# Performance work log

Measured on AMD Instinct MI355X. Metric: run time of the kernel, lower is better.

Reference implementation:

```python
import jax, jax.numpy as jnp
import numpy as np

B, N, DIM = 4, 4096, 512
HEADS, DH = 8, 64          # dim_head = dim // 8
M = 256                    # num_landmarks = dim // 2
ITERS = 6                  # pinv iterations
K = 33                     # residual depthwise conv kernel
INNER = HEADS * DH


def setup_inputs() -> dict:
    key = jax.random.key(0)
    ks = jax.random.split(key, 7)
    return {
        "x": jax.random.normal(ks[0], (B, N, DIM), jnp.float32),
        "norm_w": 1.0 + 0.02 * jax.random.normal(ks[1], (DIM,), jnp.float32),
        "norm_b": 0.02 * jax.random.normal(ks[2], (DIM,), jnp.float32),
        "w_qkv": jax.random.normal(ks[3], (DIM, 3 * INNER), jnp.float32) / np.sqrt(DIM),
        "w_out": jax.random.normal(ks[4], (INNER, DIM), jnp.float32) / np.sqrt(INNER),
        "b_out": 0.02 * jax.random.normal(ks[5], (DIM,), jnp.float32),
        "res_w": jax.random.normal(ks[6], (HEADS, 1, K, 1), jnp.float32) / np.sqrt(K),
    }


def _moore_penrose_pinv(x, iters):
    # iterative Newton-Schulz pseudoinverse, as in lucidrains nystrom-attention
    abs_x = jnp.abs(x)
    col = abs_x.sum(-1)
    row = abs_x.sum(-2)
    z = jnp.swapaxes(x, -1, -2) / (jnp.max(col) * jnp.max(row))
    I = jnp.eye(x.shape[-1], dtype=x.dtype)
    for _ in range(iters):
        xz = x @ z
        z = 0.25 * z @ (13.0 * I - xz @ (15.0 * I - xz @ (7.0 * I - xz)))
    return z


def reference(x, norm_w, norm_b, w_qkv, w_out, b_out, res_w):
    # LayerNorm (eps=1e-5, torch default)
    mu = x.mean(-1, keepdims=True)
    var = ((x - mu) ** 2).mean(-1, keepdims=True)
    xn = (x - mu) / jnp.sqrt(var + 1e-5) * norm_w + norm_b

    qkv = xn @ w_qkv                               # [B,N,3*INNER]
    q, k, v = jnp.split(qkv, 3, axis=-1)
    to_heads = lambda t: t.reshape(B, N, HEADS, DH).transpose(0, 2, 1, 3)  # [B,H,N,D]
    q, k, v = to_heads(q), to_heads(k), to_heads(v)
    q = q * (DH ** -0.5)

    # landmarks: mean over consecutive blocks of l = N // M tokens
    l = N // M
    q_l = q.reshape(B, HEADS, M, l, DH).mean(3)    # [B,H,M,D]
    k_l = k.reshape(B, HEADS, M, l, DH).mean(3)

    sim1 = jnp.einsum('bhid,bhjd->bhij', q, k_l)   # [B,H,N,M]
    sim2 = jnp.einsum('bhid,bhjd->bhij', q_l, k_l) # [B,H,M,M]
    sim3 = jnp.einsum('bhid,bhjd->bhij', q_l, k)   # [B,H,M,N]
    a1 = jax.nn.softmax(sim1, -1)
    a2 = jax.nn.softmax(sim2, -1)
    a3 = jax.nn.softmax(sim3, -1)

    a2_inv = _moore_penrose_pinv(a2, ITERS)
    out = (a1 @ a2_inv) @ (a3 @ v)                 # [B,H,N,D]

    # residual depthwise conv over sequence dim (Conv2d(h,h,(33,1),groups=h))
    out = out + jax.lax.conv_general_dilated(
        v, res_w, (1, 1), ((K // 2, K // 2), (0, 0)),
        feature_group_count=HEADS,
        dimension_numbers=('NCHW', 'OIHW', 'NCHW'))

    out = out.transpose(0, 2, 1, 3).reshape(B, N, INNER)
    out = out @ w_out + b_out                      # to_out (dropout inactive at eval)
    return x + out                                 # TransLayer residual
```

## Files before the change

kernel.cpp:

```cpp
#include <hip/hip_runtime.h>
#include <math.h>

typedef unsigned short u16;
typedef short s16x8 __attribute__((ext_vector_type(8)));
typedef float f32x4 __attribute__((ext_vector_type(4)));

#define MFMA16(a, b, c) __builtin_amdgcn_mfma_f32_16x16x32_bf16((a), (b), (c), 0, 0, 0)

__device__ __forceinline__ u16 f2b(float f) {
  unsigned u = __float_as_uint(f);
  unsigned r = (u + 0x7fff + ((u >> 16) & 1)) >> 16;
  return (u16)r;
}
__device__ __forceinline__ float b2f(u16 h) { return __uint_as_float(((unsigned)h) << 16); }

__global__ __launch_bounds__(256) void prep_kernel(const float* __restrict__ x, const float* __restrict__ w,
    const float* __restrict__ b, u16* __restrict__ xn,
    const float* __restrict__ Wq, u16* __restrict__ WqT,
    const float* __restrict__ Wo, u16* __restrict__ WoT,
    unsigned* __restrict__ scal) {
  int bI = blockIdx.x;
  int t = threadIdx.x;
  if (bI == 0 && t == 0) { scal[0] = 0u; scal[1] = 0u; }
  if (bI < 16384) {
    int row = bI;
    const float* xr = x + (size_t)row * 512;
    float v0 = xr[t], v1 = xr[t + 256];
    float s = v0 + v1, ss = v0*v0 + v1*v1;
    for (int o = 32; o > 0; o >>= 1) { s += __shfl_down(s, o); ss += __shfl_down(ss, o); }
    __shared__ float ls[4], lss[4];
    int wid = t >> 6, lane = t & 63;
    if (lane == 0) { ls[wid] = s; lss[wid] = ss; }
    __syncthreads();
    float tot  = ls[0]+ls[1]+ls[2]+ls[3];
    float tot2 = lss[0]+lss[1]+lss[2]+lss[3];
    float mean = tot * (1.f/512);
    float var  = tot2 * (1.f/512) - mean*mean;
    float inv = rsqrtf(var + 1e-5f);
    u16* xo = xn + (size_t)row * 512;
    xo[t]     = f2b((v0-mean)*inv*w[t]     + b[t]);
    xo[t+256] = f2b((v1-mean)*inv*w[t+256] + b[t+256]);
  } else if (bI < 16384 + 3072) {
    int idx = (bI - 16384)*256 + t;
    int r = idx / 1536, c = idx - r*1536;
    WqT[(size_t)c*512 + r] = f2b(Wq[idx]);
  } else {
    int idx = (bI - 19456)*256 + t;
    int r = idx >> 9, c = idx & 511;
    WoT[(size_t)c*512 + r] = f2b(Wo[idx]);
  }
}

__device__ __forceinline__ void gemm128_pf(const u16* __restrict__ A, const u16* __restrict__ BT,
    int K, int ldA, int ldBT, int row0, int col0, u16* As, u16* Bs, f32x4 acc[4][4]) {
  int t = threadIdx.x, lane = t & 63, wid = t >> 6;
  int wr = (wid >> 1) * 64, wc = (wid & 1) * 64;
  int lr = lane & 15, lg = lane >> 4;
  int sr = t >> 2, sc = (t & 3) * 8;
  const u16* Ar0 = A  + (size_t)(row0 + sr)*ldA + sc;
  const u16* Ar1 = A  + (size_t)(row0 + sr + 64)*ldA + sc;
  const u16* Br0 = BT + (size_t)(col0 + sr)*ldBT + sc;
  const u16* Br1 = BT + (size_t)(col0 + sr + 64)*ldBT + sc;
  uint4 pa0 = *(const uint4*)Ar0, pa1 = *(const uint4*)Ar1;
  uint4 pb0 = *(const uint4*)Br0, pb1 = *(const uint4*)Br1;
  for (int k0 = 0; k0 < K; k0 += 32) {
    __syncthreads();
    *(uint4*)&As[sr*40 + sc]        = pa0;
    *(uint4*)&As[(sr + 64)*40 + sc] = pa1;
    *(uint4*)&Bs[sr*40 + sc]        = pb0;
    *(uint4*)&Bs[(sr + 64)*40 + sc] = pb1;
    __syncthreads();
    if (k0 + 32 < K) {
      pa0 = *(const uint4*)(Ar0 + k0 + 32);
      pa1 = *(const uint4*)(Ar1 + k0 + 32);
      pb0 = *(const uint4*)(Br0 + k0 + 32);
      pb1 = *(const uint4*)(Br1 + k0 + 32);
    }
    s16x8 af[4], bf[4];
    #pragma unroll
    for (int f = 0; f < 4; f++) {
      af[f] = *(s16x8*)&As[(wr + f*16 + lr)*40 + lg*8];
      bf[f] = *(s16x8*)&Bs[(wc + f*16 + lr)*40 + lg*8];
    }
    #pragma unroll
    for (int i = 0; i < 4; i++)
      #pragma unroll
      for (int j = 0; j < 4; j++)
        acc[i][j] = MFMA16(af[i], bf[j], acc[i][j]);
  }
}

__device__ __forceinline__ void gemm64_pf(const u16* __restrict__ Ab, const u16* __restrict__ Bb,
    int row0, int col0, u16* As, u16* Bs, f32x4 acc[2][2]) {
  int t = threadIdx.x, lane = t & 63, wid = t >> 6;
  int wr = (wid >> 1)*32, wc = (wid & 1)*32;
  int lr = lane & 15, lg = lane >> 4;
  int sr = t >> 3, sc = (t & 7)*8;
  const u16* Ar0 = Ab + (size_t)(row0 + sr)*256 + sc;
  const u16* Ar1 = Ab + (size_t)(row0 + 32 + sr)*256 + sc;
  const u16* Br0 = Bb + (size_t)(col0 + sr)*256 + sc;
  const u16* Br1 = Bb + (size_t)(col0 + 32 + sr)*256 + sc;
  uint4 pa0 = *(const uint4*)Ar0, pa1 = *(const uint4*)Ar1;
  uint4 pb0 = *(const uint4*)Br0, pb1 = *(const uint4*)Br1;
  for (int k0 = 0; k0 < 256; k0 += 64) {
    __syncthreads();
    *(uint4*)&As[sr*72 + sc]        = pa0;
    *(uint4*)&As[(sr + 32)*72 + sc] = pa1;
    *(uint4*)&Bs[sr*72 + sc]        = pb0;
    *(uint4*)&Bs[(sr + 32)*72 + sc] = pb1;
    __syncthreads();
    if (k0 + 64 < 256) {
      pa0 = *(const uint4*)(Ar0 + k0 + 64);
      pa1 = *(const uint4*)(Ar1 + k0 + 64);
      pb0 = *(const uint4*)(Br0 + k0 + 64);
      pb1 = *(const uint4*)(Br1 + k0 + 64);
    }
    #pragma unroll
    for (int kk = 0; kk < 2; kk++) {
      s16x8 af[2], bf[2];
      #pragma unroll
      for (int f = 0; f < 2; f++) {
        af[f] = *(s16x8*)&As[(wr + f*16 + lr)*72 + kk*32 + lg*8];
        bf[f] = *(s16x8*)&Bs[(wc + f*16 + lr)*72 + kk*32 + lg*8];
      }
      #pragma unroll
      for (int i = 0; i < 2; i++)
        #pragma unroll
        for (int j = 0; j < 2; j++)
          acc[i][j] = MFMA16(af[i], bf[j], acc[i][j]);
    }
  }
}

__global__ __launch_bounds__(256, 4) void qkv_mfma(const u16* __restrict__ xn, const u16* __restrict__ wT,
    u16* __restrict__ q, u16* __restrict__ k, u16* __restrict__ v,
    u16* __restrict__ ql, u16* __restrict__ kl) {
  __shared__ u16 As[128*40], Bs[128*40];
  f32x4 acc[4][4];
  #pragma unroll
  for (int i = 0; i < 4; i++)
    #pragma unroll
    for (int j = 0; j < 4; j++) acc[i][j] = (f32x4)0.f;
  int bI = blockIdx.x;
  int job = (bI & 7)*192 + (bI >> 3);
  int row0 = (job / 12) * 128, col0 = (job % 12) * 128;
  gemm128_pf(xn, wT, 512, 512, 512, row0, col0, As, Bs, acc);
  int t = threadIdx.x, lane = t & 63, wid = t >> 6, lr = lane & 15, lg = lane >> 4;
  int wr = (wid >> 1)*64, wc = (wid & 1)*64;
  int part = col0 >> 9;
  #pragma unroll
  for (int i = 0; i < 4; i++)
    #pragma unroll
    for (int j = 0; j < 4; j++)
      #pragma unroll
      for (int r = 0; r < 4; r++) {
        int row = row0 + wr + i*16 + lg*4 + r;
        int col = col0 + wc + j*16 + lr;
        float val = acc[i][j][r];
        int rem = col & 511, h = rem >> 6, d = rem & 63;
        int b = row >> 12, n = row & 4095;
        size_t bh = (size_t)(b*8 + h);
        size_t dst = (bh*4096 + n)*64 + d;
        if (part == 0)      q[dst] = f2b(val * 0.125f);
        else if (part == 1) k[dst] = f2b(val);
        else                v[dst] = f2b(val);
      }
  if (part <= 1) {
    #pragma unroll
    for (int i = 0; i < 4; i++) {
      #pragma unroll
      for (int j = 0; j < 4; j++) {
        float s = acc[i][j][0] + acc[i][j][1] + acc[i][j][2] + acc[i][j][3];
        s += __shfl_xor(s, 16);
        s += __shfl_xor(s, 32);
        if (lg == 0) {
          int row16 = row0 + wr + i*16;
          int b = row16 >> 12, n = row16 & 4095;
          int m = n >> 4;
          int col = col0 + wc + j*16 + lr;
          int rem = col & 511, h = rem >> 6, d = rem & 63;
          size_t dst = ((size_t)(b*8 + h)*256 + m)*64 + d;
          if (part == 0) ql[dst] = f2b(s * (0.125f/16.f));
          else           kl[dst] = f2b(s * (1.f/16.f));
        }
      }
    }
  }
}

__global__ __launch_bounds__(256, 4) void out_mfma(const u16* __restrict__ outh, const u16* __restrict__ wT,
    const float* __restrict__ bo, const float* __restrict__ x, float* __restrict__ out) {
  __shared__ u16 As[128*40], Bs[128*40];
  f32x4 acc[4][4];
  #pragma unroll
  for (int i = 0; i < 4; i++)
    #pragma unroll
    for (int j = 0; j < 4; j++) acc[i][j] = (f32x4)0.f;
  int bI = blockIdx.x;
  int job = (bI & 7)*64 + (bI >> 3);
  int row0 = (job / 4) * 128, col0 = (job % 4) * 128;
  gemm128_pf(outh, wT, 512, 512, 512, row0, col0, As, Bs, acc);
  int t = threadIdx.x, lane = t & 63, wid = t >> 6, lr = lane & 15, lg = lane >> 4;
  int wr = (wid >> 1)*64, wc = (wid & 1)*64;
  #pragma unroll
  for (int i = 0; i < 4; i++)
    #pragma unroll
    for (int j = 0; j < 4; j++)
      #pragma unroll
      for (int r = 0; r < 4; r++) {
        int row = row0 + wr + i*16 + lg*4 + r;
        int col = col0 + wc + j*16 + lr;
        size_t idx = (size_t)row*512 + col;
        out[idx] = x[idx] + acc[i][j][r] + bo[col];
      }
}

__global__ __launch_bounds__(256) void mid_kernel(
    const u16* __restrict__ v, u16* __restrict__ vT,
    const u16* __restrict__ ql, const u16* __restrict__ kl,
    u16* __restrict__ a2h, float* __restrict__ pcs,
    const float* __restrict__ rw, u16* __restrict__ outh) {
  __shared__ __align__(16) u16 smem[25600];
  int bI = blockIdx.x;
  int t = threadIdx.x;
  if (bI < 128) {
    int rq = bI & 3, bh = bI >> 2;
    u16* Qs  = smem;
    u16* Ks2 = smem + 4608;
    float* wcol = (float*)(smem + 23040);
    int lane = t & 63, wid = t >> 6, lr = lane & 15, lg = lane >> 4;
    #pragma unroll
    for (int p = 0; p < 2; p++) {
      int c = t + p*256;
      int r = c >> 3, col = (c & 7)*8;
      *(uint4*)&Qs[r*72 + col] = *(const uint4*)&ql[((size_t)bh*256 + rq*64 + r)*64 + col];
    }
    #pragma unroll
    for (int p = 0; p < 8; p++) {
      int c = t + p*256;
      int r = c >> 3, col = (c & 7)*8;
      *(uint4*)&Ks2[r*72 + col] = *(const uint4*)&kl[((size_t)bh*256 + r)*64 + col];
    }
    __syncthreads();
    float colp[16];
    #pragma unroll
    for (int cf = 0; cf < 16; cf++) colp[cf] = 0.f;
    int rbase = wid*16;
    s16x8 a0 = *(s16x8*)&Qs[(rbase + lr)*72 + lg*8];
    s16x8 a1 = *(s16x8*)&Qs[(rbase + lr)*72 + 32 + lg*8];
    f32x4 sf[16];
    #pragma unroll
    for (int cf = 0; cf < 16; cf++) {
      s16x8 b0 = *(s16x8*)&Ks2[(cf*16 + lr)*72 + lg*8];
      s16x8 b1 = *(s16x8*)&Ks2[(cf*16 + lr)*72 + 32 + lg*8];
      sf[cf] = MFMA16(a1, b1, MFMA16(a0, b0, (f32x4)0.f));
    }
    #pragma unroll
    for (int r = 0; r < 4; r++) {
      float mx = -3e38f;
      #pragma unroll
      for (int cf = 0; cf < 16; cf++) mx = fmaxf(mx, sf[cf][r]);
      #pragma unroll
      for (int o = 1; o < 16; o <<= 1) mx = fmaxf(mx, __shfl_xor(mx, o));
      float sum = 0.f;
      #pragma unroll
      for (int cf = 0; cf < 16; cf++) { sf[cf][r] = __expf(sf[cf][r] - mx); sum += sf[cf][r]; }
      #pragma unroll
      for (int o = 1; o < 16; o <<= 1) sum += __shfl_xor(sum, o);
      float inv = 1.f / sum;
      int row = rq*64 + rbase + lg*4 + r;
      size_t base = (size_t)bh*65536 + (size_t)row*256;
      #pragma unroll
      for (int cf = 0; cf < 16; cf++) {
        float pp = sf[cf][r] * inv;
        a2h[base + cf*16 + lr] = f2b(pp);
        colp[cf] += pp;
      }
    }
    #pragma unroll
    for (int cf = 0; cf < 16; cf++) {
      colp[cf] += __shfl_xor(colp[cf], 16);
      colp[cf] += __shfl_xor(colp[cf], 32);
    }
    if (lg == 0) {
      #pragma unroll
      for (int cf = 0; cf < 16; cf++) wcol[wid*256 + cf*16 + lr] = colp[cf];
    }
    __syncthreads();
    pcs[((size_t)bh*4 + rq)*256 + t] = wcol[t] + wcol[256 + t] + wcol[512 + t] + wcol[768 + t];
  } else if (bI < 2176) {
    int idx = bI - 128;
    int bh = idx >> 6, n0 = (idx & 63) * 64;
    u16* tile = smem;
    const u16* vb = v + ((size_t)bh*4096 + n0)*64;
    #pragma unroll
    for (int p = 0; p < 2; p++) {
      int c = t + p*256;
      int r = c >> 3, col = (c & 7)*8;
      *(uint4*)&tile[r*72 + col] = *(const uint4*)&vb[(size_t)r*64 + col];
    }
    __syncthreads();
    #pragma unroll
    for (int p = 0; p < 2; p++) {
      int c = t + p*256;
      int d = c >> 3, ncol = (c & 7)*8;
      u16 tmp[8];
      #pragma unroll
      for (int j = 0; j < 8; j++) tmp[j] = tile[(ncol + j)*72 + d];
      *(uint4*)&vT[((size_t)bh*64 + d)*4096 + n0 + ncol] = *(uint4*)tmp;
    }
  } else {
    int idx = bI - 2176;
    int bh = idx >> 5, n0 = (idx & 31) * 128;
    int b = bh >> 3, h = bh & 7;
    u16* tile = smem;
    float* wsm = (float*)(smem + 11520);
    if (t < 33) wsm[t] = rw[h*33 + t];
    const u16* vb = v + ((size_t)bh*4096)*64;
    #pragma unroll
    for (int p = 0; p < 5; p++) {
      int c = t + p*256;
      int r = c >> 3, col = (c & 7)*8;
      int nn = n0 - 16 + r;
      uint4 val = make_uint4(0u,0u,0u,0u);
      if (nn >= 0 && nn < 4096) val = *(const uint4*)&vb[(size_t)nn*64 + col];
      *(uint4*)&tile[r*72 + col] = val;
    }
    __syncthreads();
    int d8 = (t & 7) * 8;
    int r0 = t >> 3;
    #pragma unroll
    for (int pass = 0; pass < 4; pass++) {
      int lrow = pass*32 + r0;
      float acc[8] = {};
      #pragma unroll
      for (int j = 0; j < 33; j++) {
        uint4 vv = *(uint4*)&tile[(lrow + j)*72 + d8];
        float w = wsm[j];
        acc[0] += b2f((u16)(vv.x & 0xffff)) * w;
        acc[1] += b2f((u16)(vv.x >> 16))    * w;
        acc[2] += b2f((u16)(vv.y & 0xffff)) * w;
        acc[3] += b2f((u16)(vv.y >> 16))    * w;
        acc[4] += b2f((u16)(vv.z & 0xffff)) * w;
        acc[5] += b2f((u16)(vv.z >> 16))    * w;
        acc[6] += b2f((u16)(vv.w & 0xffff)) * w;
        acc[7] += b2f((u16)(vv.w >> 16))    * w;
      }
      size_t oi = ((size_t)(b*4096 + n0 + lrow))*512 + h*64 + d8;
      uint4 nv;
      nv.x = (unsigned)f2b(acc[0]) | ((unsigned)f2b(acc[1]) << 16);
      nv.y = (unsigned)f2b(acc[2]) | ((unsigned)f2b(acc[3]) << 16);
      nv.z = (unsigned)f2b(acc[4]) | ((unsigned)f2b(acc[5]) << 16);
      nv.w = (unsigned)f2b(acc[6]) | ((unsigned)f2b(acc[7]) << 16);
      *(uint4*)&outh[oi] = nv;
    }
  }
}

__global__ __launch_bounds__(256) void fp_cm(const u16* __restrict__ Q, const u16* __restrict__ Kg,
    const u16* __restrict__ VT, u16* __restrict__ po, float* __restrict__ pl,
    const float* __restrict__ pcs, unsigned* __restrict__ scal) {
  __shared__ __align__(16) u16 smem[13824];
  int bI = blockIdx.x;
  int t = threadIdx.x;
  if (bI >= 512) {
    float* red = (float*)smem;
    int bh = bI - 512;
    size_t b4 = (size_t)bh*4*256;
    red[t] = pcs[b4 + t] + pcs[b4 + 256 + t] + pcs[b4 + 512 + t] + pcs[b4 + 768 + t];
    __syncthreads();
    for (int o = 128; o > 0; o >>= 1) {
      if (t < o) red[t] = fmaxf(red[t], red[t+o]);
      __syncthreads();
    }
    if (t == 0) atomicMax(scal + 1, __float_as_uint(red[0]));
    return;
  }
  int ch = bI & 7, qg = (bI >> 3) & 1, bh = bI >> 4;
  u16* Ks = smem;
  u16* Vs = smem + 4608;
  u16* Ps = smem + 9216;
  int lane = t & 63, wid = t >> 6, lr = lane & 15, lg = lane >> 4;
  const u16* Qb  = Q  + ((size_t)bh*256)*64;
  const u16* Kb  = Kg + ((size_t)bh*4096 + ch*512)*64;
  const u16* VTb = VT + ((size_t)bh*64)*4096 + ch*512;
  s16x8 aq[2][2];
  #pragma unroll
  for (int qq = 0; qq < 2; qq++) {
    int qrow = (qg*2 + qq)*64 + wid*16 + lr;
    aq[qq][0] = *(const s16x8*)&Qb[(size_t)qrow*64 + lg*8];
    aq[qq][1] = *(const s16x8*)&Qb[(size_t)qrow*64 + 32 + lg*8];
  }
  f32x4 oacc[2][4];
  f32x4 lacc[2];
  #pragma unroll
  for (int qq = 0; qq < 2; qq++) {
    lacc[qq] = (f32x4)0.f;
    #pragma unroll
    for (int f = 0; f < 4; f++) oacc[qq][f] = (f32x4)0.f;
  }
  u16* Pw = Ps + wid*16*72;
  uint4 pk[2], pv[2];
  #pragma unroll
  for (int p = 0; p < 2; p++) {
    int c = t + p*256; int r = c >> 3, cc = (c & 7)*8;
    pk[p] = *(const uint4*)&Kb[(size_t)r*64 + cc];
    pv[p] = *(const uint4*)&VTb[(size_t)r*4096 + cc];
  }
  for (int k0 = 0; k0 < 512; k0 += 64) {
    __syncthreads();
    #pragma unroll
    for (int p = 0; p < 2; p++) {
      int c = t + p*256; int r = c >> 3, cc = (c & 7)*8;
      *(uint4*)&Ks[r*72 + cc] = pk[p];
      *(uint4*)&Vs[r*72 + cc] = pv[p];
    }
    __syncthreads();
    if (k0 + 64 < 512) {
      #pragma unroll
      for (int p = 0; p < 2; p++) {
        int c = t + p*256; int r = c >> 3, cc = (c & 7)*8;
        pk[p] = *(const uint4*)&Kb[(size_t)(k0 + 64 + r)*64 + cc];
        pv[p] = *(const uint4*)&VTb[(size_t)r*4096 + k0 + 64 + cc];
      }
    }
    #pragma unroll
    for (int qq = 0; qq < 2; qq++) {
      f32x4 sf[4];
      #pragma unroll
      for (int f = 0; f < 4; f++) {
        s16x8 b0 = *(s16x8*)&Ks[(f*16 + lr)*72 + lg*8];
        s16x8 b1 = *(s16x8*)&Ks[(f*16 + lr)*72 + 32 + lg*8];
        f32x4 s = (f32x4)0.f;
        s = MFMA16(aq[qq][0], b0, s);
        s = MFMA16(aq[qq][1], b1, s);
        sf[f] = s;
      }
      #pragma unroll
      for (int r = 0; r < 4; r++) {
        #pragma unroll
        for (int f = 0; f < 4; f++) {
          float pv2 = __expf(sf[f][r] - 8.f);
          lacc[qq][r] += pv2;
          Pw[(lg*4 + r)*72 + f*16 + lr] = f2b(pv2);
        }
      }
      #pragma unroll
      for (int ks = 0; ks < 2; ks++) {
        s16x8 ap = *(s16x8*)&Pw[lr*72 + ks*32 + lg*8];
        #pragma unroll
        for (int df = 0; df < 4; df++) {
          s16x8 bv = *(s16x8*)&Vs[(df*16 + lr)*72 + ks*32 + lg*8];
          oacc[qq][df] = MFMA16(ap, bv, oacc[qq][df]);
        }
      }
    }
  }
  #pragma unroll
  for (int qq = 0; qq < 2; qq++) {
    #pragma unroll
    for (int r = 0; r < 4; r++) {
      float s = lacc[qq][r];
      #pragma unroll
      for (int o = 1; o < 16; o <<= 1) s += __shfl_xor(s, o);
      lacc[qq][r] = s;
    }
  }
  #pragma unroll
  for (int qq = 0; qq < 2; qq++) {
    int pidx = (bh*4 + qg*2 + qq)*8 + ch;
    #pragma unroll
    for (int r = 0; r < 4; r++) {
      int lrow = wid*16 + lg*4 + r;
      if (lr == 0) pl[pidx*64 + lrow] = lacc[qq][r];
      uint2 pw2;
      pw2.x = (unsigned)f2b(oacc[qq][0][r]) | ((unsigned)f2b(oacc[qq][1][r]) << 16);
      pw2.y = (unsigned)f2b(oacc[qq][2][r]) | ((unsigned)f2b(oacc[qq][3][r]) << 16);
      *(uint2*)&po[((size_t)pidx*64 + lrow)*64 + lr*4] = pw2;
    }
  }
}

__global__ __launch_bounds__(256) void merge_z0(const u16* __restrict__ po,
    const float* __restrict__ pl, u16* __restrict__ a3vT,
    const u16* __restrict__ a2h, const unsigned* __restrict__ scal,
    u16* __restrict__ zA, u16* __restrict__ zAT) {
  __shared__ u16 tile[64*72];
  int bI = blockIdx.x;
  int t = threadIdx.x;
  if (bI < 128) {
    int qt = bI & 3, bh = bI >> 2;
    int lrow = t & 63, dg = t >> 6;
    int pbase = (bh*4 + qt)*8;
    float L = 0.f;
    #pragma unroll
    for (int ch = 0; ch < 8; ch++) L += pl[(pbase+ch)*64 + lrow];
    float Oacc[16];
    #pragma unroll
    for (int ss = 0; ss < 16; ss++) Oacc[ss] = 0.f;
    #pragma unroll
    for (int ch = 0; ch < 8; ch++) {
      const u16* pr = &po[(((size_t)(pbase+ch)*64 + lrow)*64) + dg*16];
      uint4 v0 = *(const uint4*)pr;
      uint4 v1 = *(const uint4*)(pr + 8);
      unsigned arr[8] = {v0.x, v0.y, v0.z, v0.w, v1.x, v1.y, v1.z, v1.w};
      #pragma unroll
      for (int jj = 0; jj < 8; jj++) {
        Oacc[jj*2]   += b2f((u16)(arr[jj] & 0xffff));
        Oacc[jj*2+1] += b2f((u16)(arr[jj] >> 16));
      }
    }
    float Linv = 1.f / L;
    #pragma unroll
    for (int ss = 0; ss < 16; ss++) {
      int s = dg*16 + ss;
      int c = ((s & 3) << 4) | (s >> 2);
      tile[c*72 + lrow] = f2b(Oacc[ss] * Linv);
    }
    __syncthreads();
    #pragma unroll
    for (int p = 0; p < 2; p++) {
      int idx = t + p*256;
      int d = idx >> 3, seg = idx & 7;
      u16 tmp[8];
      #pragma unroll
      for (int j = 0; j < 8; j++) tmp[j] = tile[d*72 + seg*8 + j];
      *(uint4*)&a3vT[((size_t)bh*64 + d)*256 + qt*64 + seg*8] = *(uint4*)tmp;
    }
  } else {
    size_t idx = (size_t)(bI - 128)*256 + t;
    float inv = 1.f / __uint_as_float(scal[1]);
    size_t bh = idx >> 16; int rem = (int)(idx & 65535); int i = rem >> 8, j = rem & 255;
    zA[idx]  = f2b(b2f(a2h[(bh<<16) + ((size_t)j<<8) + i]) * inv);
    zAT[idx] = f2b(b2f(a2h[idx]) * inv);
  }
}

__global__ __launch_bounds__(256) void pinv_s1(const u16* __restrict__ a2h, const u16* __restrict__ zcT,
    u16* __restrict__ xz, u16* __restrict__ xzT, u16* __restrict__ e1T) {
  __shared__ u16 As[64*72], Bs[64*72];
  size_t bb = (size_t)blockIdx.z << 16;
  f32x4 acc[2][2];
  #pragma unroll
  for (int i = 0; i < 2; i++) { acc[i][0] = (f32x4)0.f; acc[i][1] = (f32x4)0.f; }
  int row0 = blockIdx.y*64, col0 = blockIdx.x*64;
  gemm64_pf(a2h + bb, zcT + bb, row0, col0, As, Bs, acc);
  int t = threadIdx.x, lane = t & 63, wid = t >> 6, lr = lane & 15, lg = lane >> 4;
  int wr = (wid >> 1)*32, wc = (wid & 1)*32;
  #pragma unroll
  for (int i = 0; i < 2; i++)
    #pragma unroll
    for (int j = 0; j < 2; j++)
      #pragma unroll
      for (int r = 0; r < 4; r++) {
        int row = row0 + wr + i*16 + lg*4 + r;
        int col = col0 + wc + j*16 + lr;
        float c = acc[i][j][r];
        xz [bb + (size_t)row*256 + col] = f2b(c);
        xzT[bb + (size_t)col*256 + row] = f2b(c);
        e1T[bb + (size_t)col*256 + row] = f2b((row == col ? 7.f : 0.f) - c);
      }
}

__global__ __launch_bounds__(256) void pinv_s2(const u16* __restrict__ xz, const u16* __restrict__ e1T,
    const u16* __restrict__ zc, const u16* __restrict__ xzT,
    u16* __restrict__ e2T, u16* __restrict__ W) {
  __shared__ u16 As[64*72], Bs[64*72];
  int bz = blockIdx.z;
  bool isQ = bz < 32;
  size_t bb = (size_t)(isQ ? bz : bz - 32) << 16;
  const u16* Aptr = (isQ ? xz : zc) + bb;
  const u16* Bptr = (isQ ? e1T : xzT) + bb;
  f32x4 acc[2][2];
  #pragma unroll
  for (int i = 0; i < 2; i++) { acc[i][0] = (f32x4)0.f; acc[i][1] = (f32x4)0.f; }
  int row0 = blockIdx.y*64, col0 = blockIdx.x*64;
  gemm64_pf(Aptr, Bptr, row0, col0, As, Bs, acc);
  int t = threadIdx.x, lane = t & 63, wid = t >> 6, lr = lane & 15, lg = lane >> 4;
  int wr = (wid >> 1)*32, wc = (wid & 1)*32;
  #pragma unroll
  for (int i = 0; i < 2; i++)
    #pragma unroll
    for (int j = 0; j < 2; j++)
      #pragma unroll
      for (int r = 0; r < 4; r++) {
        int row = row0 + wr + i*16 + lg*4 + r;
        int col = col0 + wc + j*16 + lr;
        float c = acc[i][j][r];
        if (isQ) e2T[bb + (size_t)col*256 + row] = f2b((row == col ? 15.f : 0.f) - c);
        else     W  [bb + (size_t)row*256 + col] = f2b(c);
      }
}

__global__ __launch_bounds__(256) void pinv_s3(const u16* __restrict__ W, const u16* __restrict__ e2T,
    const u16* __restrict__ zc, u16* __restrict__ zn, u16* __restrict__ znT) {
  __shared__ u16 As[64*72], Bs[64*72];
  size_t bb = (size_t)blockIdx.z << 16;
  f32x4 acc[2][2];
  #pragma unroll
  for (int i = 0; i < 2; i++) { acc[i][0] = (f32x4)0.f; acc[i][1] = (f32x4)0.f; }
  int row0 = blockIdx.y*64, col0 = blockIdx.x*64;
  gemm64_pf(W + bb, e2T + bb, row0, col0, As, Bs, acc);
  int t = threadIdx.x, lane = t & 63, wid = t >> 6, lr = lane & 15, lg = lane >> 4;
  int wr = (wid >> 1)*32, wc = (wid & 1)*32;
  #pragma unroll
  for (int i = 0; i < 2; i++)
    #pragma unroll
    for (int j = 0; j < 2; j++)
      #pragma unroll
      for (int r = 0; r < 4; r++) {
        int row = row0 + wr + i*16 + lg*4 + r;
        int col = col0 + wc + j*16 + lr;
        size_t idx = bb + (size_t)row*256 + col;
        float val = 3.25f*b2f(zc[idx]) - 0.25f*acc[i][j][r];
        zn [idx] = f2b(val);
        znT[bb + (size_t)col*256 + row] = f2b(val);
      }
}

__global__ __launch_bounds__(256) void bmm64(const u16* __restrict__ A, const u16* __restrict__ BT,
    u16* __restrict__ CT, int M, int N, int K) {
  __shared__ u16 As[64*40], Bs[64*40];
  int batch = blockIdx.z;
  const u16* Ab = A  + (size_t)batch*M*K;
  const u16* Bb = BT + (size_t)batch*N*K;
  int row0 = blockIdx.y*64, col0 = blockIdx.x*64;
  int t = threadIdx.x, lane = t & 63, wid = t >> 6, lr = lane & 15, lg = lane >> 4;
  int wr = (wid >> 1)*32, wc = (wid & 1)*32;
  int sr = t >> 2, sc = (t & 3)*8;
  const u16* Arow = Ab + (size_t)(row0 + sr)*K + sc;
  const u16* Brow = Bb + (size_t)(col0 + sr)*K + sc;
  uint4 pa = *(const uint4*)Arow;
  uint4 pb = *(const uint4*)Brow;
  f32x4 acc[2][2];
  #pragma unroll
  for (int i = 0; i < 2; i++)
    #pragma unroll
    for (int j = 0; j < 2; j++) acc[i][j] = (f32x4)0.f;
  for (int k0 = 0; k0 < K; k0 += 32) {
    __syncthreads();
    *(uint4*)&As[sr*40 + sc] = pa;
    *(uint4*)&Bs[sr*40 + sc] = pb;
    __syncthreads();
    if (k0 + 32 < K) {
      pa = *(const uint4*)(Arow + k0 + 32);
      pb = *(const uint4*)(Brow + k0 + 32);
    }
    s16x8 af[2], bf[2];
    #pragma unroll
    for (int f = 0; f < 2; f++) {
      af[f] = *(s16x8*)&As[(wr + f*16 + lr)*40 + lg*8];
      bf[f] = *(s16x8*)&Bs[(wc + f*16 + lr)*40 + lg*8];
    }
    #pragma unroll
    for (int i = 0; i < 2; i++)
      #pragma unroll
      for (int j = 0; j < 2; j++)
        acc[i][j] = MFMA16(af[i], bf[j], acc[i][j]);
  }
  size_t cb = (size_t)batch*M*N;
  #pragma unroll
  for (int i = 0; i < 2; i++)
    #pragma unroll
    for (int j = 0; j < 2; j++)
      #pragma unroll
      for (int r = 0; r < 4; r++) {
        int row = row0 + wr + i*16 + lg*4 + r;
        int col = col0 + wc + j*16 + lr;
        CT[cb + (size_t)col*M + row] = f2b(acc[i][j][r]);
      }
}

__global__ __launch_bounds__(256, 4) void flash_a1(const u16* __restrict__ Q, const u16* __restrict__ Kl,
    const u16* __restrict__ W2T, u16* __restrict__ outh) {
  __shared__ u16 Ks[64*72];
  __shared__ u16 Vs[64*264];
  __shared__ u16 Ps[4*16*264];
  int bh = blockIdx.y;
  int q0 = blockIdx.x * 64;
  int t = threadIdx.x, lane = t & 63, wid = t >> 6, lr = lane & 15, lg = lane >> 4;
  const u16* Qb = Q + ((size_t)bh*4096)*64;
  #pragma unroll
  for (int p = 0; p < 8; p++) {
    int c = t + p*256; int r = c >> 5, col = (c & 31)*8;
    *(uint4*)&Vs[r*264 + col] = *(const uint4*)&W2T[((size_t)bh*64 + r)*256 + col];
  }
  int qrow = q0 + wid*16 + lr;
  s16x8 aq0 = *(const s16x8*)&Qb[(size_t)qrow*64 + lg*8];
  s16x8 aq1 = *(const s16x8*)&Qb[(size_t)qrow*64 + 32 + lg*8];
  f32x4 sf[16];
  #pragma unroll
  for (int f = 0; f < 16; f++) sf[f] = (f32x4)0.f;
  #pragma unroll
  for (int kt = 0; kt < 4; kt++) {
    __syncthreads();
    #pragma unroll
    for (int p = 0; p < 2; p++) {
      int c = t + p*256; int r = c >> 3, cc = (c & 7)*8;
      *(uint4*)&Ks[r*72 + cc] = *(const uint4*)&Kl[((size_t)bh*256 + kt*64 + r)*64 + cc];
    }
    __syncthreads();
    #pragma unroll
    for (int f2 = 0; f2 < 4; f2++) {
      s16x8 b0 = *(s16x8*)&Ks[(f2*16 + lr)*72 + lg*8];
      s16x8 b1 = *(s16x8*)&Ks[(f2*16 + lr)*72 + 32 + lg*8];
      sf[kt*4 + f2] = MFMA16(aq1, b1, MFMA16(aq0, b0, sf[kt*4 + f2]));
    }
  }
  u16* Pw = Ps + wid*16*264;
  float linv[4];
  #pragma unroll
  for (int r = 0; r < 4; r++) {
    float sum = 0.f;
    #pragma unroll
    for (int f = 0; f < 16; f++) {
      float pv = __expf(sf[f][r] - 8.f);
      sum += pv;
      Pw[(lg*4 + r)*264 + f*16 + lr] = f2b(pv);
    }
    #pragma unroll
    for (int o = 1; o < 16; o <<= 1) sum += __shfl_xor(sum, o);
    linv[r] = 1.f / sum;
  }
  f32x4 oacc[4];
  #pragma unroll
  for (int f = 0; f < 4; f++) oacc[f] = (f32x4)0.f;
  #pragma unroll
  for (int ks = 0; ks < 8; ks++) {
    s16x8 ap = *(s16x8*)&Pw[lr*264 + ks*32 + lg*8];
    #pragma unroll
    for (int df = 0; df < 4; df++) {
      s16x8 bv = *(s16x8*)&Vs[(df*16 + lr)*264 + ks*32 + lg*8];
      oacc[df] = MFMA16(ap, bv, oacc[df]);
    }
  }
  int b = bh >> 3, h = bh & 7;
  #pragma unroll
  for (int df = 0; df < 4; df++)
    #pragma unroll
    for (int r = 0; r < 4; r++) {
      int lrow = wid*16 + lg*4 + r;
      int col = df*16 + lr;
      size_t oi = ((size_t)(b*4096 + q0 + lrow))*512 + h*64 + col;
      outh[oi] = f2b(b2f(outh[oi]) + oacc[df][r] * linv[r]);
    }
}

extern "C" void kernel_launch(void* const* d_in, const int* in_sizes, int n_in,
                              void* d_out, int out_size, void* d_ws, size_t ws_size,
                              hipStream_t stream) {
  const float* x      = (const float*)d_in[0];
  const float* norm_w = (const float*)d_in[1];
  const float* norm_b = (const float*)d_in[2];
  const float* w_qkv  = (const float*)d_in[3];
  const float* w_out  = (const float*)d_in[4];
  const float* b_out  = (const float*)d_in[5];
  const float* res_w  = (const float*)d_in[6];
  float* out = (float*)d_out;
  char* ws = (char*)d_ws;

  size_t off = 0;
  u16* xn    = (u16*)(ws + off); off += 16777216;
  u16* q     = (u16*)(ws + off); off += 16777216;
  u16* k     = (u16*)(ws + off); off += 16777216;
  u16* v     = (u16*)(ws + off); off += 16777216;
  u16* vT    = (u16*)(ws + off); off += 16777216;
  u16* ql    = (u16*)(ws + off); off += 1048576;
  u16* kl    = (u16*)(ws + off); off += 1048576;
  u16* a2h   = (u16*)(ws + off); off += 4194304;
  u16* zA    = (u16*)(ws + off); off += 4194304;
  u16* zAT   = (u16*)(ws + off); off += 4194304;
  u16* zB    = (u16*)(ws + off); off += 4194304;
  u16* zBT   = (u16*)(ws + off); off += 4194304;
  u16* xz    = (u16*)(ws + off); off += 4194304;
  u16* xzT   = (u16*)(ws + off); off += 4194304;
  u16* e1T   = (u16*)(ws + off); off += 4194304;
  u16* e2T   = (u16*)(ws + off); off += 4194304;
  u16* Wm    = (u16*)(ws + off); off += 4194304;
  u16* a3vT  = (u16*)(ws + off); off += 1048576;
  u16* w2T   = (u16*)(ws + off); off += 1048576;
  u16* wqkvT = (u16*)(ws + off); off += 1572864;
  u16* woutT = (u16*)(ws + off); off += 524288;
  u16* outh  = (u16*)(ws + off); off += 16777216;
  u16* po    = (u16*)(ws + off); off += 8388608;
  float* pl  = (float*)(ws + off); off += 262144;
  float* pcs = (float*)(ws + off); off += 131072;
  unsigned* scal = (unsigned*)(ws + off); off += 8;

  prep_kernel<<<20480, 256, 0, stream>>>(x, norm_w, norm_b, xn, w_qkv, wqkvT, w_out, woutT, scal);
  qkv_mfma<<<1536, 256, 0, stream>>>(xn, wqkvT, q, k, v, ql, kl);
  mid_kernel<<<3200, 256, 0, stream>>>(v, vT, ql, kl, a2h, pcs, res_w, outh);
  fp_cm<<<544, 256, 0, stream>>>(ql, k, vT, po, pl, pcs, scal);
  merge_z0<<<8320, 256, 0, stream>>>(po, pl, a3vT, a2h, scal, zA, zAT);

  u16 *zc = zA, *zcT = zAT, *zn = zB, *znT = zBT;
  for (int it = 0; it < 6; it++) {
    pinv_s1<<<dim3(4,4,32), 256, 0, stream>>>(a2h, zcT, xz, xzT, e1T);
    pinv_s2<<<dim3(4,4,64), 256, 0, stream>>>(xz, e1T, zc, xzT, e2T, Wm);
    pinv_s3<<<dim3(4,4,32), 256, 0, stream>>>(Wm, e2T, zc, zn, znT);
    u16* tp;
    tp = zc; zc = zn; zn = tp;
    tp = zcT; zcT = znT; znT = tp;
  }

  bmm64<<<dim3(1,4,32), 256, 0, stream>>>(zc, a3vT, w2T, 256, 64, 256);
  flash_a1<<<dim3(64, 32), 256, 0, stream>>>(q, kl, w2T, outh);
  out_mfma<<<512, 256, 0, stream>>>(outh, woutT, b_out, x, out);
}
```

Measured before the change: 383.8 us.

## Fold z0 scaling into pinv stages and overlap flash/merge with pinv launches

Writes the transposed landmark softmax directly from mid_kernel and applies the 1/(max col*max row) scale inside the first pinv iteration, removing the merge_z0 elementwise pass. The a3·v partial flash blocks and their merge are fused as extra blocks into the first two pinv_s1 launches, so that independent work fills the otherwise underused GPU during the small pinv GEMMs. The column-max reduction moves to its own tiny kernel. This adds mode branching and larger shared-memory footprints to pinv_s1.

```diff
diff --git a/kernel.cpp b/kernel.cpp
--- a/kernel.cpp
+++ b/kernel.cpp
@@ -218,7 +218,7 @@
 __global__ __launch_bounds__(256) void mid_kernel(
     const u16* __restrict__ v, u16* __restrict__ vT,
     const u16* __restrict__ ql, const u16* __restrict__ kl,
-    u16* __restrict__ a2h, float* __restrict__ pcs,
+    u16* __restrict__ a2h, u16* __restrict__ a2hT, float* __restrict__ pcs,
     const float* __restrict__ rw, u16* __restrict__ outh) {
   __shared__ __align__(16) u16 smem[25600];
   int bI = blockIdx.x;
@@ -227,6 +227,7 @@
     int rq = bI & 3, bh = bI >> 2;
     u16* Qs  = smem;
     u16* Ks2 = smem + 4608;
+    u16* Pt  = smem;
     float* wcol = (float*)(smem + 23040);
     int lane = t & 63, wid = t >> 6, lr = lane & 15, lg = lane >> 4;
     #pragma unroll
@@ -255,6 +256,7 @@
       s16x8 b1 = *(s16x8*)&Ks2[(cf*16 + lr)*72 + 32 + lg*8];
       sf[cf] = MFMA16(a1, b1, MFMA16(a0, b0, (f32x4)0.f));
     }
+    float invs[4];
     #pragma unroll
     for (int r = 0; r < 4; r++) {
       float mx = -3e38f;
@@ -268,6 +270,7 @@
       #pragma unroll
       for (int o = 1; o < 16; o <<= 1) sum += __shfl_xor(sum, o);
       float inv = 1.f / sum;
+      invs[r] = inv;
       int row = rq*64 + rbase + lg*4 + r;
       size_t base = (size_t)bh*65536 + (size_t)row*256;
       #pragma unroll
@@ -288,6 +291,22 @@
     }
     __syncthreads();
     pcs[((size_t)bh*4 + rq)*256 + t] = wcol[t] + wcol[256 + t] + wcol[512 + t] + wcol[768 + t];
+    #pragma unroll
+    for (int cf = 0; cf < 16; cf++) {
+      int col = cf*16 + lr;
+      #pragma unroll
+      for (int r = 0; r < 4; r++) {
+        int lrow = rbase + lg*4 + r;
+        Pt[col*72 + lrow] = f2b(sf[cf][r] * invs[r]);
+      }
+    }
+    __syncthreads();
+    #pragma unroll
+    for (int p = 0; p < 8; p++) {
+      int c = t + p*256;
+      int j = c >> 3, o8 = (c & 7)*8;
+      *(uint4*)&a2hT[(size_t)bh*65536 + (size_t)j*256 + rq*64 + o8] = *(uint4*)&Pt[j*72 + o8];
+    }
   } else if (bI < 2176) {
     int idx = bI - 128;
     int bh = idx >> 6, n0 = (idx & 63) * 64;
@@ -357,29 +376,53 @@
   }
 }
 
-__global__ __launch_bounds__(256) void fp_cm(const u16* __restrict__ Q, const u16* __restrict__ Kg,
-    const u16* __restrict__ VT, u16* __restrict__ po, float* __restrict__ pl,
-    const float* __restrict__ pcs, unsigned* __restrict__ scal) {
-  __shared__ __align__(16) u16 smem[13824];
-  int bI = blockIdx.x;
-  int t = threadIdx.x;
-  if (bI >= 512) {
-    float* red = (float*)smem;
-    int bh = bI - 512;
-    size_t b4 = (size_t)bh*4*256;
-    red[t] = pcs[b4 + t] + pcs[b4 + 256 + t] + pcs[b4 + 512 + t] + pcs[b4 + 768 + t];
-    __syncthreads();
-    for (int o = 128; o > 0; o >>= 1) {
-      if (t < o) red[t] = fmaxf(red[t], red[t+o]);
-      __syncthreads();
-    }
-    if (t == 0) atomicMax(scal + 1, __float_as_uint(red[0]));
-    return;
-  }
-  int ch = bI & 7, qg = (bI >> 3) & 1, bh = bI >> 4;
+__global__ __launch_bounds__(256) void colmax_kernel(const float* __restrict__ pcs, unsigned* __restrict__ scal) {
+  __shared__ float red[256];
+  int bh = blockIdx.x, t = threadIdx.x;
+  size_t b4 = (size_t)bh*4*256;
+  red[t] = pcs[b4 + t] + pcs[b4 + 256 + t] + pcs[b4 + 512 + t] + pcs[b4 + 768 + t];
+  __syncthreads();
+  for (int o = 128; o > 0; o >>= 1) {
+    if (t < o) red[t] = fmaxf(red[t], red[t+o]);
+    __syncthreads();
+  }
+  if (t == 0) atomicMax(scal + 1, __float_as_uint(red[0]));
+}
+
+__device__ __forceinline__ void s1_body(int bI, u16* As, u16* Bs,
+    const u16* __restrict__ a2h, const u16* __restrict__ zcT,
+    u16* __restrict__ xz, u16* __restrict__ xzT, u16* __restrict__ e1T, float sc) {
+  size_t bb = (size_t)(bI >> 4) << 16;
+  int row0 = ((bI >> 2) & 3)*64, col0 = (bI & 3)*64;
+  f32x4 acc[2][2];
+  #pragma unroll
+  for (int i = 0; i < 2; i++) { acc[i][0] = (f32x4)0.f; acc[i][1] = (f32x4)0.f; }
+  gemm64_pf(a2h + bb, zcT + bb, row0, col0, As, Bs, acc);
+  int t = threadIdx.x, lane = t & 63, wid = t >> 6, lr = lane & 15, lg = lane >> 4;
+  int wr = (wid >> 1)*32, wc = (wid & 1)*32;
+  #pragma unroll
+  for (int i = 0; i < 2; i++)
+    #pragma unroll
+    for (int j = 0; j < 2; j++)
+      #pragma unroll
+      for (int r = 0; r < 4; r++) {
+        int row = row0 + wr + i*16 + lg*4 + r;
+        int col = col0 + wc + j*16 + lr;
+        float c = acc[i][j][r] * sc;
+        xz [bb + (size_t)row*256 + col] = f2b(c);
+        xzT[bb + (size_t)col*256 + row] = f2b(c);
+        e1T[bb + (size_t)col*256 + row] = f2b((row == col ? 7.f : 0.f) - c);
+      }
+}
+
+__device__ __forceinline__ void flash_body(int f, u16* smem,
+    const u16* __restrict__ Q, const u16* __restrict__ Kg, const u16* __restrict__ VT,
+    u16* __restrict__ po, float* __restrict__ pl) {
   u16* Ks = smem;
   u16* Vs = smem + 4608;
   u16* Ps = smem + 9216;
+  int t = threadIdx.x;
+  int ch = f & 7, qg = (f >> 3) & 1, bh = f >> 4;
   int lane = t & 63, wid = t >> 6, lr = lane & 15, lg = lane >> 4;
   const u16* Qb  = Q  + ((size_t)bh*256)*64;
   const u16* Kb  = Kg + ((size_t)bh*4096 + ch*512)*64;
@@ -397,7 +440,7 @@
   for (int qq = 0; qq < 2; qq++) {
     lacc[qq] = (f32x4)0.f;
     #pragma unroll
-    for (int f = 0; f < 4; f++) oacc[qq][f] = (f32x4)0.f;
+    for (int ff = 0; ff < 4; ff++) oacc[qq][ff] = (f32x4)0.f;
   }
   u16* Pw = Ps + wid*16*72;
   uint4 pk[2], pv[2];
@@ -428,21 +471,21 @@
     for (int qq = 0; qq < 2; qq++) {
       f32x4 sf[4];
       #pragma unroll
-      for (int f = 0; f < 4; f++) {
-        s16x8 b0 = *(s16x8*)&Ks[(f*16 + lr)*72 + lg*8];
-        s16x8 b1 = *(s16x8*)&Ks[(f*16 + lr)*72 + 32 + lg*8];
+      for (int ff = 0; ff < 4; ff++) {
+        s16x8 b0 = *(s16x8*)&Ks[(ff*16 + lr)*72 + lg*8];
+        s16x8 b1 = *(s16x8*)&Ks[(ff*16 + lr)*72 + 32 + lg*8];
         f32x4 s = (f32x4)0.f;
         s = MFMA16(aq[qq][0], b0, s);
         s = MFMA16(aq[qq][1], b1, s);
-        sf[f] = s;
+        sf[ff] = s;
       }
       #pragma unroll
       for (int r = 0; r < 4; r++) {
         #pragma unroll
-        for (int f = 0; f < 4; f++) {
-          float pv2 = __expf(sf[f][r] - 8.f);
+        for (int ff = 0; ff < 4; ff++) {
+          float pv2 = __expf(sf[ff][r] - 8.f);
           lacc[qq][r] += pv2;
-          Pw[(lg*4 + r)*72 + f*16 + lr] = f2b(pv2);
+          Pw[(lg*4 + r)*72 + ff*16 + lr] = f2b(pv2);
         }
       }
       #pragma unroll
@@ -481,90 +524,71 @@
   }
 }
 
-__global__ __launch_bounds__(256) void merge_z0(const u16* __restrict__ po,
-    const float* __restrict__ pl, u16* __restrict__ a3vT,
-    const u16* __restrict__ a2h, const unsigned* __restrict__ scal,
-    u16* __restrict__ zA, u16* __restrict__ zAT) {
-  __shared__ u16 tile[64*72];
+__device__ __forceinline__ void merge_body(int m, u16* tile,
+    const u16* __restrict__ po, const float* __restrict__ pl, u16* __restrict__ a3vT) {
+  int t = threadIdx.x;
+  int qt = m & 3, bh = m >> 2;
+  int lrow = t & 63, dg = t >> 6;
+  int pbase = (bh*4 + qt)*8;
+  float L = 0.f;
+  #pragma unroll
+  for (int ch = 0; ch < 8; ch++) L += pl[(pbase+ch)*64 + lrow];
+  float Oacc[16];
+  #pragma unroll
+  for (int ss = 0; ss < 16; ss++) Oacc[ss] = 0.f;
+  #pragma unroll
+  for (int ch = 0; ch < 8; ch++) {
+    const u16* pr = &po[(((size_t)(pbase+ch)*64 + lrow)*64) + dg*16];
+    uint4 v0 = *(const uint4*)pr;
+    uint4 v1 = *(const uint4*)(pr + 8);
+    unsigned arr[8] = {v0.x, v0.y, v0.z, v0.w, v1.x, v1.y, v1.z, v1.w};
+    #pragma unroll
+    for (int jj = 0; jj < 8; jj++) {
+      Oacc[jj*2]   += b2f((u16)(arr[jj] & 0xffff));
+      Oacc[jj*2+1] += b2f((u16)(arr[jj] >> 16));
+    }
+  }
+  float Linv = 1.f / L;
+  #pragma unroll
+  for (int ss = 0; ss < 16; ss++) {
+    int s = dg*16 + ss;
+    int c = ((s & 3) << 4) | (s >> 2);
+    tile[c*72 + lrow] = f2b(Oacc[ss] * Linv);
+  }
+  __syncthreads();
+  #pragma unroll
+  for (int p = 0; p < 2; p++) {
+    int idx = t + p*256;
+    int d = idx >> 3, seg = idx & 7;
+    u16 tmp[8];
+    #pragma unroll
+    for (int j = 0; j < 8; j++) tmp[j] = tile[d*72 + seg*8 + j];
+    *(uint4*)&a3vT[((size_t)bh*64 + d)*256 + qt*64 + seg*8] = *(uint4*)tmp;
+  }
+}
+
+__global__ __launch_bounds__(256) void pinv_s1_f(int mode,
+    const u16* __restrict__ a2h, const u16* __restrict__ zcT,
+    u16* __restrict__ xz, u16* __restrict__ xzT, u16* __restrict__ e1T,
+    const unsigned* __restrict__ scal,
+    const u16* __restrict__ Q, const u16* __restrict__ Kg, const u16* __restrict__ VT,
+    u16* __restrict__ po, float* __restrict__ pl, u16* __restrict__ a3vT) {
+  __shared__ __align__(16) u16 smem[13824];
   int bI = blockIdx.x;
-  int t = threadIdx.x;
-  if (bI < 128) {
-    int qt = bI & 3, bh = bI >> 2;
-    int lrow = t & 63, dg = t >> 6;
-    int pbase = (bh*4 + qt)*8;
-    float L = 0.f;
-    #pragma unroll
-    for (int ch = 0; ch < 8; ch++) L += pl[(pbase+ch)*64 + lrow];
-    float Oacc[16];
-    #pragma unroll
-    for (int ss = 0; ss < 16; ss++) Oacc[ss] = 0.f;
-    #pragma unroll
-    for (int ch = 0; ch < 8; ch++) {
-      const u16* pr = &po[(((size_t)(pbase+ch)*64 + lrow)*64) + dg*16];
-      uint4 v0 = *(const uint4*)pr;
-      uint4 v1 = *(const uint4*)(pr + 8);
-      unsigned arr[8] = {v0.x, v0.y, v0.z, v0.w, v1.x, v1.y, v1.z, v1.w};
-      #pragma unroll
-      for (int jj = 0; jj < 8; jj++) {
-        Oacc[jj*2]   += b2f((u16)(arr[jj] & 0xffff));
-        Oacc[jj*2+1] += b2f((u16)(arr[jj] >> 16));
-      }
-    }
-    float Linv = 1.f / L;
-    #pragma unroll
-    for (int ss = 0; ss < 16; ss++) {
-      int s = dg*16 + ss;
-      int c = ((s & 3) << 4) | (s >> 2);
-      tile[c*72 + lrow] = f2b(Oacc[ss] * Linv);
-    }
-    __syncthreads();
-    #pragma unroll
-    for (int p = 0; p < 2; p++) {
-      int idx = t + p*256;
-      int d = idx >> 3, seg = idx & 7;
-      u16 tmp[8];
-      #pragma unroll
-      for (int j = 0; j < 8; j++) tmp[j] = tile[d*72 + seg*8 + j];
-      *(uint4*)&a3vT[((size_t)bh*64 + d)*256 + qt*64 + seg*8] = *(uint4*)tmp;
-    }
+  if (bI < 512) {
+    float sc = (mode == 1) ? 1.f/__uint_as_float(scal[1]) : 1.f;
+    s1_body(bI, smem, smem + 4608, a2h, zcT, xz, xzT, e1T, sc);
+  } else if (mode == 1) {
+    flash_body(bI - 512, smem, Q, Kg, VT, po, pl);
   } else {
-    size_t idx = (size_t)(bI - 128)*256 + t;
-    float inv = 1.f / __uint_as_float(scal[1]);
-    size_t bh = idx >> 16; int rem = (int)(idx & 65535); int i = rem >> 8, j = rem & 255;
-    zA[idx]  = f2b(b2f(a2h[(bh<<16) + ((size_t)j<<8) + i]) * inv);
-    zAT[idx] = f2b(b2f(a2h[idx]) * inv);
-  }
-}
-
-__global__ __launch_bounds__(256) void pinv_s1(const u16* __restrict__ a2h, const u16* __restrict__ zcT,
-    u16* __restrict__ xz, u16* __restrict__ xzT, u16* __restrict__ e1T) {
-  __shared__ u16 As[64*72], Bs[64*72];
-  size_t bb = (size_t)blockIdx.z << 16;
-  f32x4 acc[2][2];
-  #pragma unroll
-  for (int i = 0; i < 2; i++) { acc[i][0] = (f32x4)0.f; acc[i][1] = (f32x4)0.f; }
-  int row0 = blockIdx.y*64, col0 = blockIdx.x*64;
-  gemm64_pf(a2h + bb, zcT + bb, row0, col0, As, Bs, acc);
-  int t = threadIdx.x, lane = t & 63, wid = t >> 6, lr = lane & 15, lg = lane >> 4;
-  int wr = (wid >> 1)*32, wc = (wid & 1)*32;
-  #pragma unroll
-  for (int i = 0; i < 2; i++)
-    #pragma unroll
-    for (int j = 0; j < 2; j++)
-      #pragma unroll
-      for (int r = 0; r < 4; r++) {
-        int row = row0 + wr + i*16 + lg*4 + r;
-        int col = col0 + wc + j*16 + lr;
-        float c = acc[i][j][r];
-        xz [bb + (size_t)row*256 + col] = f2b(c);
-        xzT[bb + (size_t)col*256 + row] = f2b(c);
-        e1T[bb + (size_t)col*256 + row] = f2b((row == col ? 7.f : 0.f) - c);
-      }
+    merge_body(bI - 512, smem, po, pl, a3vT);
+  }
 }
 
 __global__ __launch_bounds__(256) void pinv_s2(const u16* __restrict__ xz, const u16* __restrict__ e1T,
     const u16* __restrict__ zc, const u16* __restrict__ xzT,
-    u16* __restrict__ e2T, u16* __restrict__ W) {
+    u16* __restrict__ e2T, u16* __restrict__ W,
+    const unsigned* __restrict__ scal, int useInv) {
   __shared__ u16 As[64*72], Bs[64*72];
   int bz = blockIdx.z;
   bool isQ = bz < 32;
@@ -576,6 +600,7 @@
   for (int i = 0; i < 2; i++) { acc[i][0] = (f32x4)0.f; acc[i][1] = (f32x4)0.f; }
   int row0 = blockIdx.y*64, col0 = blockIdx.x*64;
   gemm64_pf(Aptr, Bptr, row0, col0, As, Bs, acc);
+  float scw = useInv ? 1.f/__uint_as_float(scal[1]) : 1.f;
   int t = threadIdx.x, lane = t & 63, wid = t >> 6, lr = lane & 15, lg = lane >> 4;
   int wr = (wid >> 1)*32, wc = (wid & 1)*32;
   #pragma unroll
@@ -588,12 +613,13 @@
         int col = col0 + wc + j*16 + lr;
         float c = acc[i][j][r];
         if (isQ) e2T[bb + (size_t)col*256 + row] = f2b((row == col ? 15.f : 0.f) - c);
-        else     W  [bb + (size_t)row*256 + col] = f2b(c);
+        else     W  [bb + (size_t)row*256 + col] = f2b(c * scw);
       }
 }
 
 __global__ __launch_bounds__(256) void pinv_s3(const u16* __restrict__ W, const u16* __restrict__ e2T,
-    const u16* __restrict__ zc, u16* __restrict__ zn, u16* __restrict__ znT) {
+    const u16* __restrict__ zc, u16* __restrict__ zn, u16* __restrict__ znT,
+    const unsigned* __restrict__ scal, int useInv) {
   __shared__ u16 As[64*72], Bs[64*72];
   size_t bb = (size_t)blockIdx.z << 16;
   f32x4 acc[2][2];
@@ -601,6 +627,7 @@
   for (int i = 0; i < 2; i++) { acc[i][0] = (f32x4)0.f; acc[i][1] = (f32x4)0.f; }
   int row0 = blockIdx.y*64, col0 = blockIdx.x*64;
   gemm64_pf(W + bb, e2T + bb, row0, col0, As, Bs, acc);
+  float zsc = useInv ? 3.25f/__uint_as_float(scal[1]) : 3.25f;
   int t = threadIdx.x, lane = t & 63, wid = t >> 6, lr = lane & 15, lg = lane >> 4;
   int wr = (wid >> 1)*32, wc = (wid & 1)*32;
   #pragma unroll
@@ -612,7 +639,7 @@
         int row = row0 + wr + i*16 + lg*4 + r;
         int col = col0 + wc + j*16 + lr;
         size_t idx = bb + (size_t)row*256 + col;
-        float val = 3.25f*b2f(zc[idx]) - 0.25f*acc[i][j][r];
+        float val = zsc*b2f(zc[idx]) - 0.25f*acc[i][j][r];
         zn [idx] = f2b(val);
         znT[bb + (size_t)col*256 + row] = f2b(val);
       }
@@ -789,21 +816,25 @@
 
   prep_kernel<<<20480, 256, 0, stream>>>(x, norm_w, norm_b, xn, w_qkv, wqkvT, w_out, woutT, scal);
   qkv_mfma<<<1536, 256, 0, stream>>>(xn, wqkvT, q, k, v, ql, kl);
-  mid_kernel<<<3200, 256, 0, stream>>>(v, vT, ql, kl, a2h, pcs, res_w, outh);
-  fp_cm<<<544, 256, 0, stream>>>(ql, k, vT, po, pl, pcs, scal);
-  merge_z0<<<8320, 256, 0, stream>>>(po, pl, a3vT, a2h, scal, zA, zAT);
-
+  mid_kernel<<<3200, 256, 0, stream>>>(v, vT, ql, kl, a2h, zA, pcs, res_w, outh);
+  colmax_kernel<<<32, 256, 0, stream>>>(pcs, scal);
+
+  pinv_s1_f<<<1024, 256, 0, stream>>>(1, a2h, a2h, xz, xzT, e1T, scal, ql, k, vT, po, pl, a3vT);
+  pinv_s2<<<dim3(4,4,64), 256, 0, stream>>>(xz, e1T, zA, xzT, e2T, Wm, scal, 1);
+  pinv_s3<<<dim3(4,4,32), 256, 0, stream>>>(Wm, e2T, zA, zB, zBT, scal, 1);
+  pinv_s1_f<<<640, 256, 0, stream>>>(2, a2h, zBT, xz, xzT, e1T, scal, ql, k, vT, po, pl, a3vT);
+  pinv_s2<<<dim3(4,4,64), 256, 0, stream>>>(xz, e1T, zB, xzT, e2T, Wm, scal, 0);
+  pinv_s3<<<dim3(4,4,32), 256, 0, stream>>>(Wm, e2T, zB, zA, zAT, scal, 0);
   u16 *zc = zA, *zcT = zAT, *zn = zB, *znT = zBT;
-  for (int it = 0; it < 6; it++) {
-    pinv_s1<<<dim3(4,4,32), 256, 0, stream>>>(a2h, zcT, xz, xzT, e1T);
-    pinv_s2<<<dim3(4,4,64), 256, 0, stream>>>(xz, e1T, zc, xzT, e2T, Wm);
-    pinv_s3<<<dim3(4,4,32), 256, 0, stream>>>(Wm, e2T, zc, zn, znT);
+  for (int it = 0; it < 4; it++) {
+    pinv_s1_f<<<512, 256, 0, stream>>>(0, a2h, zcT, xz, xzT, e1T, scal, ql, k, vT, po, pl, a3vT);
+    pinv_s2<<<dim3(4,4,64), 256, 0, stream>>>(xz, e1T, zc, xzT, e2T, Wm, scal, 0);
+    pinv_s3<<<dim3(4,4,32), 256, 0, stream>>>(Wm, e2T, zc, zn, znT, scal, 0);
     u16* tp;
     tp = zc; zc = zn; zn = tp;
     tp = zcT; zcT = znT; znT = tp;
   }
-
-  bmm64<<<dim3(1,4,32), 256, 0, stream>>>(zc, a3vT, w2T, 256, 64, 256);
+  bmm64<<<dim3(1,4,32), 256, 0, stream>>>(zA, a3vT, w2T, 256, 64, 256);
   flash_a1<<<dim3(64, 32), 256, 0, stream>>>(q, kl, w2T, outh);
   out_mfma<<<512, 256, 0, stream>>>(outh, woutT, b_out, x, out);
 }
```

Result: no change. 387.0 us (+0.8%).
